# Performance work log

Hardware: AMD Instinct MI355X
Metric: run time of the kernel (lower is better)

Reference implementation:

```python
import jax, jax.numpy as jnp
import numpy as np
import math

B, S, D = 4, 2048, 1024
TAU = 0.5

def setup_inputs() -> dict:
    key = jax.random.key(0)
    ks = jax.random.split(key, 10)
    s = 1.0 / math.sqrt(D)
    return {
        "node_emb": jax.random.normal(ks[0], (B, S, D), jnp.float32),
        "label_emb": jax.random.normal(ks[1], (B, S, D), jnp.float32),
        "Wq": jax.random.uniform(ks[2], (D, D), jnp.float32, -s, s),
        "bq": jax.random.uniform(ks[3], (D,), jnp.float32, -s, s),
        "Wk": jax.random.uniform(ks[4], (D, D), jnp.float32, -s, s),
        "bk": jax.random.uniform(ks[5], (D,), jnp.float32, -s, s),
        "Wv": jax.random.uniform(ks[6], (D, D), jnp.float32, -s, s),
        "bv": jax.random.uniform(ks[7], (D,), jnp.float32, -s, s),
        "Wp": jax.random.uniform(ks[8], (D, D), jnp.float32, -s, s),
        "bp": jax.random.uniform(ks[9], (D,), jnp.float32, -s, s),
    }

def reference(node_emb, label_emb, Wq, bq, Wk, bk, Wv, bv, Wp, bp):
    # Q from label_emb; K, V from node_emb (torch Linear: x @ W.T + b)
    Q = label_emb @ Wq.T + bq          # [B, S, D]
    K = node_emb @ Wk.T + bk           # [B, S, D]
    V = node_emb @ Wv.T + bv           # [B, S, D]
    d = node_emb.shape[-1]
    score = jnp.einsum('bqd,bkd->bqk', Q, K) / jnp.sqrt(jnp.float32(d))
    # causal (lower-triangular) mask, masked_fill(-1e9) BEFORE the tau scale
    causal = jnp.tril(jnp.ones((score.shape[-2], score.shape[-1]), bool))
    score = jnp.where(causal[None, :, :], score, jnp.float32(-1e9))
    attn = jax.nn.softmax(score * TAU, axis=-1)  # [B, S, S]
    # proj_drop is Dropout(0.1); reference runs in eval mode (identity)
    z = jnp.einsum('bqk,bkd->bqd', attn, V)
    return z @ Wp.T + bp
```

## Files before the change

kernel.cpp:

```cpp
#include <hip/hip_runtime.h>
#include <hip/hip_bf16.h>
#include <stdint.h>

using bf16 = __hip_bfloat16;
typedef __bf16 bf16x8 __attribute__((ext_vector_type(8)));
typedef float f32x4 __attribute__((ext_vector_type(4)));
typedef unsigned short u16x8 __attribute__((ext_vector_type(8)));
typedef unsigned short u16x4 __attribute__((ext_vector_type(4)));

#define AS1 __attribute__((address_space(1)))
#define AS3 __attribute__((address_space(3)))

__device__ inline unsigned short f2b(float f) {
    union { __hip_bfloat16 h; unsigned short u; } cv;
    cv.h = __float2bfloat16(f);
    return cv.u;
}

__global__ __launch_bounds__(256) void cvt6(
    const float* __restrict__ i0, const float* __restrict__ i1,
    const float* __restrict__ i2, const float* __restrict__ i3,
    const float* __restrict__ i4, const float* __restrict__ i5,
    u16x8* __restrict__ o0, u16x8* __restrict__ o1,
    u16x8* __restrict__ o2, u16x8* __restrict__ o3,
    u16x8* __restrict__ o4, u16x8* __restrict__ o5,
    long nbig, long nsmall)
{
    const int y = blockIdx.y;
    const float* in = y == 0 ? i0 : (y == 1 ? i1 : (y == 2 ? i2 : (y == 3 ? i3 : (y == 4 ? i4 : i5))));
    u16x8* out = y == 0 ? o0 : (y == 1 ? o1 : (y == 2 ? o2 : (y == 3 ? o3 : (y == 4 ? o4 : o5))));
    const long n8 = (y < 2) ? nbig : nsmall;
    long i = (long)blockIdx.x * blockDim.x + threadIdx.x;
    const long stride = (long)gridDim.x * blockDim.x;
    const float4* in4 = (const float4*)in;
    for (; i < n8; i += stride) {
        float4 x = in4[2 * i], z = in4[2 * i + 1];
        u16x8 o;
        o[0] = f2b(x.x); o[1] = f2b(x.y); o[2] = f2b(x.z); o[3] = f2b(x.w);
        o[4] = f2b(z.x); o[5] = f2b(z.y); o[6] = f2b(z.z); o[7] = f2b(z.w);
        out[i] = o;
    }
}

template <typename T> __device__ inline void storev(T* p, float v);
template <> __device__ inline void storev<float>(float* p, float v) { *p = v; }
template <> __device__ inline void storev<bf16>(bf16* p, float v) { *p = __float2bfloat16(v); }

template <typename OutT, int MODE>
__global__ __launch_bounds__(512, 2) void gemmX(
    const bf16* __restrict__ A0, const bf16* __restrict__ A1,
    const bf16* __restrict__ B0p, const bf16* __restrict__ B1p,
    OutT* __restrict__ C0, OutT* __restrict__ C1,
    const float* __restrict__ bias0, const float* __restrict__ bias1,
    float scale, int lda, int ldb, int ldc, int Kdim,
    long sA, long sB, long sC)
{
    __shared__ __align__(16) char lds[131072];

    const int nwg = gridDim.x;
    const int bid = blockIdx.x;
    const int s = (nwg & 7) ? bid : ((bid & 7) * (nwg >> 3) + (bid >> 3));

    int bm, ccol0, rowB0, seg = 0, bn_s = 0, zidx = 0;
    const bf16 *A, *B;
    OutT* C;
    const float* bias = nullptr;

    if constexpr (MODE == 0) {
        bm = s >> 3; const int bnl = s & 7; seg = bnl >> 2;
        A = A0; B = B0p; rowB0 = bnl * 256;
        C = seg ? C1 : C0; bias = seg ? bias1 : bias0;
        ccol0 = (bnl & 3) * 256;
    } else if constexpr (MODE == 1) {
        seg = s >> 7; const int r = s & 127; bm = r >> 2; const int bn = r & 3;
        A = seg ? A1 : A0; B = seg ? B1p : B0p;
        C = seg ? C1 : C0; bias = seg ? nullptr : bias0;
        rowB0 = bn * 256; ccol0 = bn * 256;
    } else {
        const int z = s / 36, f = s % 36;
        int m = 0;
        while ((m + 1) * (m + 2) / 2 <= f) ++m;
        bm = m; const int bn = f - m * (m + 1) / 2;
        bn_s = bn; zidx = z;
        A = A0 + (long)z * sA; B = B0p + (long)z * sB; C = C0 + (long)z * sC;
        rowB0 = bn * 256; ccol0 = bn * 256;
    }

    const int KT = Kdim >> 6;
    const int NIT = KT >> 1;

    const int tid = threadIdx.x;
    const int lane = tid & 63;
    const int w = tid >> 6;
    const int wm = w >> 2;
    const int wn = w & 3;

    const int rowA0 = bm * 256;

    const int rr  = tid >> 3;
    const int lch = (tid & 7) ^ (rr & 7);
    const bf16* gAt = A + (long)(rowA0 + rr) * lda + lch * 8;
    const bf16* gBt = B + (long)(rowB0 + rr) * ldb + lch * 8;

#define LA(b) (lds + (b) * 65536)
#define LB(b) (lds + 32768 + (b) * 65536)

    auto SG2 = [&](const bf16* g, int ld, char* dst) {
        __builtin_amdgcn_global_load_lds((const AS1 void*)g,
            (AS3 void*)(dst + tid * 16), 16, 0, 0);
        __builtin_amdgcn_global_load_lds((const AS1 void*)(g + (long)64 * ld),
            (AS3 void*)(dst + 8192 + tid * 16), 16, 0, 0);
    };
    auto ST_A = [&](int kt, int half, int b) {
        SG2(gAt + (long)kt * 64 + (long)half * 128 * lda, lda, LA(b) + half * 16384);
    };
    auto ST_B = [&](int kt, int half, int b) {
        SG2(gBt + (long)kt * 64 + (long)half * 128 * ldb, ldb, LB(b) + half * 16384);
    };

    const int abase = (wm * 128 + (lane & 15)) * 128;
    const int bbase = (wn * 64 + (lane & 15)) * 128;
    const int cc0 = (((lane >> 4) << 4)) ^ ((lane & 7) << 4);
    const int cc1 = cc0 ^ 64;

#define RAF(b, mh, mi, kk) (*(const bf16x8*)(LA(b) + abase + (mh)*8192 + (mi)*2048 + ((kk) ? cc1 : cc0)))
#define RBF(b, ni, kk)     (*(const bf16x8*)(LB(b) + bbase + (ni)*2048 + ((kk) ? cc1 : cc0)))

    f32x4 acc[8][4] = {};
    bf16x8 ar[4][2], blo[2][2], bhi[2][2];

#define RD_A2(b, mh, MI0) { ar[MI0][0] = RAF(b, mh, MI0, 0); ar[MI0][1] = RAF(b, mh, MI0, 1); \
                            ar[(MI0)+1][0] = RAF(b, mh, (MI0)+1, 0); ar[(MI0)+1][1] = RAF(b, mh, (MI0)+1, 1); }
#define RD_BLO(b)   { blo[0][0] = RBF(b, 0, 0); blo[0][1] = RBF(b, 0, 1); blo[1][0] = RBF(b, 1, 0); blo[1][1] = RBF(b, 1, 1); }
#define RD_BHI(b)   { bhi[0][0] = RBF(b, 2, 0); bhi[0][1] = RBF(b, 2, 1); bhi[1][0] = RBF(b, 3, 0); bhi[1][1] = RBF(b, 3, 1); }

#define MQ1(MI, bb, MH, NB) { \
    f32x4 t0_ = acc[(MH)*4 + (MI)][(NB)]; \
    t0_ = __builtin_amdgcn_mfma_f32_16x16x32_bf16(ar[MI][0], bb[0][0], t0_, 0, 0, 0); \
    t0_ = __builtin_amdgcn_mfma_f32_16x16x32_bf16(ar[MI][1], bb[0][1], t0_, 0, 0, 0); \
    acc[(MH)*4 + (MI)][(NB)] = t0_; \
    f32x4 t1_ = acc[(MH)*4 + (MI)][(NB) + 1]; \
    t1_ = __builtin_amdgcn_mfma_f32_16x16x32_bf16(ar[MI][0], bb[1][0], t1_, 0, 0, 0); \
    t1_ = __builtin_amdgcn_mfma_f32_16x16x32_bf16(ar[MI][1], bb[1][1], t1_, 0, 0, 0); \
    acc[(MH)*4 + (MI)][(NB) + 1] = t1_; }

#define SCHEDB __builtin_amdgcn_sched_barrier(0)
#define BSYNC { SCHEDB; __builtin_amdgcn_s_barrier(); SCHEDB; }

    auto PRIO1 = [&]() { __builtin_amdgcn_s_setprio(1); };
    auto PRIO0 = [&]() { __builtin_amdgcn_s_setprio(0); };

    ST_A(0, 0, 0); ST_A(0, 1, 0); ST_B(0, 0, 0); ST_B(0, 1, 0);
    ST_B(1, 0, 1); ST_B(1, 1, 1);
    asm volatile("s_waitcnt vmcnt(4)" ::: "memory");
    BSYNC;
    RD_BLO(0); RD_A2(0, 0, 0); RD_A2(0, 0, 2);

    for (int i = 0; i < NIT; ++i) {
        const int t0 = 2 * i;
        const bool last = (i == NIT - 1);

        ST_A(t0 + 1, 0, 1);
        BSYNC; PRIO1();
        RD_BHI(0);
        MQ1(0, blo, 0, 0); MQ1(1, blo, 0, 0); MQ1(2, blo, 0, 0); MQ1(3, blo, 0, 0);
        PRIO0();

        ST_A(t0 + 1, 1, 1);
        BSYNC; PRIO1();
        MQ1(0, bhi, 0, 2); MQ1(1, bhi, 0, 2); MQ1(2, bhi, 0, 2); MQ1(3, bhi, 0, 2);
        RD_A2(0, 1, 0); RD_A2(0, 1, 2);
        PRIO0();

        BSYNC; PRIO1();
        MQ1(0, bhi, 1, 2); MQ1(1, bhi, 1, 2); MQ1(2, bhi, 1, 2); MQ1(3, bhi, 1, 2);
        PRIO0();

        if (!last) { ST_B(t0 + 2, 0, 0); ST_B(t0 + 2, 1, 0);
                     asm volatile("s_waitcnt vmcnt(4)" ::: "memory"); }
        else       { asm volatile("s_waitcnt vmcnt(0)" ::: "memory"); }
        BSYNC; PRIO1();
        MQ1(0, blo, 1, 0); MQ1(1, blo, 1, 0); MQ1(2, blo, 1, 0); MQ1(3, blo, 1, 0);
        RD_BLO(1); RD_A2(1, 0, 0); RD_A2(1, 0, 2);
        PRIO0();

        if (!last) ST_A(t0 + 2, 0, 0);
        BSYNC; PRIO1();
        RD_BHI(1);
        MQ1(0, blo, 0, 0); MQ1(1, blo, 0, 0); MQ1(2, blo, 0, 0); MQ1(3, blo, 0, 0);
        PRIO0();

        if (!last) ST_A(t0 + 2, 1, 0);
        BSYNC; PRIO1();
        MQ1(0, bhi, 0, 2); MQ1(1, bhi, 0, 2); MQ1(2, bhi, 0, 2); MQ1(3, bhi, 0, 2);
        RD_A2(1, 1, 0); RD_A2(1, 1, 2);
        PRIO0();

        BSYNC; PRIO1();
        MQ1(0, bhi, 1, 2); MQ1(1, bhi, 1, 2); MQ1(2, bhi, 1, 2); MQ1(3, bhi, 1, 2);
        PRIO0();

        if (!last) { ST_B(t0 + 3, 0, 1); ST_B(t0 + 3, 1, 1);
                     asm volatile("s_waitcnt vmcnt(4)" ::: "memory"); }
        BSYNC; PRIO1();
        MQ1(0, blo, 1, 0); MQ1(1, blo, 1, 0); MQ1(2, blo, 1, 0); MQ1(3, blo, 1, 0);
        if (!last) { RD_BLO(0); RD_A2(0, 0, 0); RD_A2(0, 0, 2); }
        PRIO0();
    }

    char* tw = lds + w * 16384;
    if constexpr (MODE == 2) {
        const int q = lane >> 4, t = lane & 15;
        const bool diag = (bm == bn_s);
#pragma unroll
        for (int mi = 0; mi < 8; ++mi)
#pragma unroll
            for (int ni = 0; ni < 4; ++ni)
#pragma unroll
                for (int j = 0; j < 4; ++j) {
                    float e = __expf(acc[mi][ni][j] * scale);
                    if (diag) {
                        const int rl = wm * 128 + mi * 16 + q * 4 + j;
                        const int cl = wn * 64 + t + ni * 16;
                        if (cl > rl) e = 0.f;
                    }
                    e = __bfloat162float(__float2bfloat16(e));
                    acc[mi][ni][j] = e;
                }
        float* part = (float*)C1 + ((((long)zidx * 8 + bm) * 32) + bn_s * 4 + wn) * 256;
#pragma unroll
        for (int mi = 0; mi < 8; ++mi) {
            float rs0 = acc[mi][0][0] + acc[mi][1][0] + acc[mi][2][0] + acc[mi][3][0];
            float rs1 = acc[mi][0][1] + acc[mi][1][1] + acc[mi][2][1] + acc[mi][3][1];
            float rs2 = acc[mi][0][2] + acc[mi][1][2] + acc[mi][2][2] + acc[mi][3][2];
            float rs3 = acc[mi][0][3] + acc[mi][1][3] + acc[mi][2][3] + acc[mi][3][3];
#pragma unroll
            for (int d = 1; d < 16; d <<= 1) {
                rs0 += __shfl_xor(rs0, d); rs1 += __shfl_xor(rs1, d);
                rs2 += __shfl_xor(rs2, d); rs3 += __shfl_xor(rs3, d);
            }
            if (t == mi) {
                float4 o; o.x = rs0; o.y = rs1; o.z = rs2; o.w = rs3;
                *(float4*)(part + wm * 128 + mi * 16 + q * 4) = o;
            }
        }
    }
    if (MODE == 1 && seg == 1) {
#pragma unroll
        for (int ni = 0; ni < 4; ++ni) {
            const int cl = ni * 16 + (lane & 15);
            const int sw = 8 * (cl & 7);
#pragma unroll
            for (int mi = 0; mi < 8; ++mi) {
                const int rlb = mi * 16 + ((lane >> 4) << 2);
                u16x4 o;
                o[0] = f2b(acc[mi][ni][0]); o[1] = f2b(acc[mi][ni][1]);
                o[2] = f2b(acc[mi][ni][2]); o[3] = f2b(acc[mi][ni][3]);
                *(u16x4*)(tw + cl * 256 + 2 * (rlb ^ sw)) = o;
            }
        }
        asm volatile("s_waitcnt lgkmcnt(0)" ::: "memory");
        __builtin_amdgcn_sched_barrier(0);
        const int m0 = rowA0 + wm * 128;
        const int z2 = m0 >> 11, mr = m0 & 2047;
        bf16* CT = (bf16*)C + (long)z2 * 2097152 + (long)(ccol0 + wn * 64 + lane) * 2048 + mr;
        const char* tr = tw + lane * 256;
        const int sw2 = lane & 7;
#pragma unroll
        for (int rb = 0; rb < 16; ++rb) {
            u16x8 v = *(const u16x8*)(tr + 16 * (rb ^ sw2));
            *(u16x8*)(CT + 8 * rb) = v;
        }
    } else {
        const float sc2 = (MODE == 2) ? 1.0f : scale;
        const int q = lane >> 4, t = lane & 15;
        const int c0 = ccol0 + wn * 64 + t;
#pragma unroll
        for (int mi = 0; mi < 8; ++mi) {
            char* tm = tw + mi * 2048;
#pragma unroll
            for (int ni = 0; ni < 4; ++ni) {
                const float bv = bias ? bias[c0 + ni * 16] : 0.0f;
                const int cb = (t + 16 * ni) * 2;
#pragma unroll
                for (int j = 0; j < 4; ++j) {
                    const int rl = q * 4 + j;
                    *(bf16*)(tm + rl * 128 + (cb ^ ((rl & 7) << 4))) =
                        __float2bfloat16(acc[mi][ni][j] * sc2 + bv);
                }
            }
        }
        asm volatile("s_waitcnt lgkmcnt(0)" ::: "memory");
        __builtin_amdgcn_sched_barrier(0);
        const int rr2 = lane >> 2, chb = (lane & 3) * 2;
        const int gr0 = rowA0 + wm * 128;
        bf16* Cb = (bf16*)C;
        const int gcb = ccol0 + wn * 64;
#pragma unroll
        for (int mi = 0; mi < 8; ++mi) {
            const char* tm = tw + mi * 2048;
            const long gr = gr0 + mi * 16 + rr2;
#pragma unroll
            for (int k = 0; k < 2; ++k) {
                const int chunk = chb + k;
                u16x8 v = *(const u16x8*)(tm + rr2 * 128 + ((chunk << 4) ^ ((rr2 & 7) << 4)));
                *(u16x8*)(Cb + gr * (long)ldc + gcb + chunk * 8) = v;
            }
        }
    }
#undef RAF
#undef RBF
#undef RD_A2
#undef RD_BLO
#undef RD_BHI
#undef MQ1
#undef LA
#undef LB
}

__global__ __launch_bounds__(512, 2) void pv_bal(
    const bf16* __restrict__ P, const bf16* __restrict__ VT,
    const float* __restrict__ part, float* __restrict__ out,
    const float* __restrict__ bias)
{
    __shared__ __align__(16) char lds[99328];
    float* invl = (float*)(lds + 98304);

    const int nwg = gridDim.x;
    const int bid = blockIdx.x;
    const int s = (bid & 7) * (nwg >> 3) + (bid >> 3);
    const int z = s >> 6, r = s & 63;
    const int pr = r >> 3, bn = r & 7;
    const int bmA = pr, bmB = 15 - pr;

    const bf16* Pz = P + (long)z * 2048 * 2048;
    const bf16* Vz = VT + (long)z * 1024 * 2048;

    const int tid = threadIdx.x;
    const int lane = tid & 63;
    const int w = tid >> 6;
    const int wm = w >> 2, wn = w & 3;
    const int rr = tid >> 3;
    const int lch = (tid & 7) ^ (rr & 7);

    if (tid < 256) {
        const int half = tid >> 7, rloc = tid & 127;
        const int grow = (half ? bmB : bmA) * 128 + rloc;
        const int b256 = grow >> 8, rin = grow & 255;
        const float* pp = part + (((long)z * 8 + b256) * 32) * 256 + rin;
        const int n4 = 4 * (b256 + 1);
        float s0 = 0.f, s1 = 0.f, s2 = 0.f, s3 = 0.f;
        int b4 = 0;
        for (; b4 + 4 <= n4; b4 += 4) {
            s0 += pp[(long)b4 * 256];       s1 += pp[(long)(b4 + 1) * 256];
            s2 += pp[(long)(b4 + 2) * 256]; s3 += pp[(long)(b4 + 3) * 256];
        }
        for (; b4 < n4; ++b4) s0 += pp[(long)b4 * 256];
        invl[tid] = 1.0f / ((s0 + s1) + (s2 + s3));
    }

    const bf16* gBt = Vz + (long)(bn * 128 + rr) * 2048 + lch * 8;
    const bf16* gAtA = Pz + (long)(bmA * 128 + rr) * 2048 + lch * 8;
    const bf16* gAtB = Pz + (long)(bmB * 128 + rr) * 2048 + lch * 8;

    auto SG2 = [&](const bf16* g, char* dst) {
        __builtin_amdgcn_global_load_lds((const AS1 void*)g,
            (AS3 void*)(dst + tid * 16), 16, 0, 0);
        __builtin_amdgcn_global_load_lds((const AS1 void*)(g + (long)64 * 2048),
            (AS3 void*)(dst + 8192 + tid * 16), 16, 0, 0);
    };
    auto ST = [&](const bf16* gAt, int kt, int b) {
        SG2(gAt + (long)kt * 64, lds + b * 32768);
        SG2(gBt + (long)kt * 64, lds + b * 32768 + 16384);
    };

    const int abase0 = (wm * 64 + (lane & 15)) * 128;
    const int bbase0 = 16384 + (wn * 32 + (lane & 15)) * 128;
    const int cc0 = ((lane >> 4) << 4) ^ ((lane & 7) << 4);
    const int cc1 = cc0 ^ 64;

    f32x4 acc[4][2];
    bf16x8 ar[4][2], br[2][2];

    auto RDF = [&](int t) {
        const char* base = lds + (t % 3) * 32768;
#pragma unroll
        for (int mi = 0; mi < 4; ++mi) {
            ar[mi][0] = *(const bf16x8*)(base + abase0 + mi * 2048 + cc0);
            ar[mi][1] = *(const bf16x8*)(base + abase0 + mi * 2048 + cc1);
        }
#pragma unroll
        for (int ni = 0; ni < 2; ++ni) {
            br[ni][0] = *(const bf16x8*)(base + bbase0 + ni * 2048 + cc0);
            br[ni][1] = *(const bf16x8*)(base + bbase0 + ni * 2048 + cc1);
        }
    };
    auto MFMA16 = [&]() {
#pragma unroll
        for (int mi = 0; mi < 4; ++mi)
#pragma unroll
            for (int ni = 0; ni < 2; ++ni) {
                f32x4 t_ = acc[mi][ni];
                t_ = __builtin_amdgcn_mfma_f32_16x16x32_bf16(ar[mi][0], br[ni][0], t_, 0, 0, 0);
                t_ = __builtin_amdgcn_mfma_f32_16x16x32_bf16(ar[mi][1], br[ni][1], t_, 0, 0, 0);
                acc[mi][ni] = t_;
            }
    };
    auto ZERO = [&]() {
#pragma unroll
        for (int mi = 0; mi < 4; ++mi)
#pragma unroll
            for (int ni = 0; ni < 2; ++ni) acc[mi][ni] = f32x4{0.f, 0.f, 0.f, 0.f};
    };
    auto tile_pass = [&](const bf16* gAt, int KT) {
        RDF(0);
        for (int t = 0; t < KT; ++t) {
            if (t + 2 < KT) {
                ST(gAt, t + 2, (t + 2) % 3);
                asm volatile("s_waitcnt vmcnt(4)" ::: "memory");
            } else if (t + 1 < KT) {
                asm volatile("s_waitcnt vmcnt(0)" ::: "memory");
            }
            asm volatile("s_waitcnt lgkmcnt(0)" ::: "memory");
            __builtin_amdgcn_sched_barrier(0);
            __builtin_amdgcn_s_barrier();
            __builtin_amdgcn_sched_barrier(0);
            __builtin_amdgcn_s_setprio(1);
            MFMA16();
            if (t + 1 < KT) RDF(t + 1);
            __builtin_amdgcn_s_setprio(0);
        }
    };
    auto epi = [&](int bm, int invoff) {
        const int q = lane >> 4, t16 = lane & 15;
        const int c0 = bn * 128 + wn * 32 + t16;
        float* op = out + ((long)z * 2048 + (long)bm * 128) * 1024;
#pragma unroll
        for (int mi = 0; mi < 4; ++mi)
#pragma unroll
            for (int j = 0; j < 4; ++j) {
                const int rl = wm * 64 + mi * 16 + q * 4 + j;
                const float iv = invl[invoff + rl];
#pragma unroll
                for (int ni = 0; ni < 2; ++ni) {
                    const int c = c0 + ni * 16;
                    op[(long)rl * 1024 + c] = acc[mi][ni][j] * iv + bias[c];
                }
            }
    };

    const int KTA = 2 * (bmA + 1), KTB = 2 * (bmB + 1);

    ST(gAtA, 0, 0); ST(gAtA, 1, 1);
    asm volatile("s_waitcnt vmcnt(4)" ::: "memory");
    __builtin_amdgcn_s_barrier();
    __builtin_amdgcn_sched_barrier(0);
    ZERO();
    tile_pass(gAtA, KTA);

    ST(gAtB, 0, 0); ST(gAtB, 1, 1);
    epi(bmA, 0);
    asm volatile("s_waitcnt vmcnt(0)" ::: "memory");
    __builtin_amdgcn_s_barrier();
    __builtin_amdgcn_sched_barrier(0);
    ZERO();
    tile_pass(gAtB, KTB);
    epi(bmB, 128);
}

extern "C" void kernel_launch(void* const* d_in, const int* in_sizes, int n_in,
                              void* d_out, int out_size, void* d_ws, size_t ws_size,
                              hipStream_t stream) {
    const int B = 4, S = 2048, D = 1024;
    const long MD = (long)B * S * D;
    const float scale = 0.5f / 32.0f;

    const float* node  = (const float*)d_in[0];
    const float* label = (const float*)d_in[1];
    const float* Wq = (const float*)d_in[2];
    const float* bq = (const float*)d_in[3];
    const float* Wk = (const float*)d_in[4];
    const float* bk = (const float*)d_in[5];
    const float* Wv = (const float*)d_in[6];
    const float* bv = (const float*)d_in[7];
    const float* Wp = (const float*)d_in[8];
    const float* bp = (const float*)d_in[9];
    float* out = (float*)d_out;

    char* ws = (char*)d_ws;
    bf16* nodeb  = (bf16*)(ws);
    bf16* VTb    = nodeb;
    bf16* labelb = (bf16*)(ws + 16777216);
    bf16* Wqb = (bf16*)(ws + 33554432);
    bf16* Wkb = (bf16*)(ws + 35651584);
    bf16* Wvb = (bf16*)(ws + 37748736);
    bf16* Wpb = (bf16*)(ws + 39845888);
    bf16* Qb  = (bf16*)(ws + 41943040);
    bf16* Kb  = (bf16*)(ws + 58720256);
    bf16* Vb  = (bf16*)(ws + 75497472);
    float* partial = (float*)(ws + 75497472);
    bf16* SP  = (bf16*)(ws + 92274688);
    if (ws_size < 125829120UL) return;

    cvt6<<<dim3(512, 6), 256, 0, stream>>>(
        node, label, Wq, Wk, Wv, Wp,
        (u16x8*)nodeb, (u16x8*)labelb, (u16x8*)Wqb, (u16x8*)Wkb, (u16x8*)Wvb, (u16x8*)Wpb,
        MD / 8, (long)D * D / 8);

    gemmX<bf16, 0><<<256, 512, 0, stream>>>(
        nodeb, nullptr, Wkb, nullptr, Kb, Vb, bk, bv,
        1.0f, D, D, D, D, 0, 0, 0);

    gemmX<bf16, 1><<<256, 512, 0, stream>>>(
        labelb, Vb, Wqb, Wpb, Qb, VTb, bq, nullptr,
        1.0f, D, D, D, D, 0, 0, 0);

    gemmX<bf16, 2><<<144, 512, 0, stream>>>(
        Qb, nullptr, Kb, (bf16*)nullptr, SP, (bf16*)partial, nullptr, nullptr,
        scale, D, D, S, D, (long)S * D, (long)S * D, (long)S * S);

    pv_bal<<<256, 512, 0, stream>>>(SP, VTb, partial, out, bp);
}
```

Measured before the change: 152.2 us.

## Replace causal score GEMM with dedicated 256x128-tile kernel over 288 blocks

Measured after the change: 160.6 us. 5.6% more time.

```diff
diff --git a/kernel.cpp b/kernel.cpp
--- a/kernel.cpp
+++ b/kernel.cpp
@@ -61,7 +61,7 @@
     const int bid = blockIdx.x;
     const int s = (nwg & 7) ? bid : ((bid & 7) * (nwg >> 3) + (bid >> 3));
 
-    int bm, ccol0, rowB0, seg = 0, bn_s = 0, zidx = 0;
+    int bm, ccol0, rowB0, seg = 0;
     const bf16 *A, *B;
     OutT* C;
     const float* bias = nullptr;
@@ -71,18 +71,10 @@
         A = A0; B = B0p; rowB0 = bnl * 256;
         C = seg ? C1 : C0; bias = seg ? bias1 : bias0;
         ccol0 = (bnl & 3) * 256;
-    } else if constexpr (MODE == 1) {
+    } else {
         seg = s >> 7; const int r = s & 127; bm = r >> 2; const int bn = r & 3;
         A = seg ? A1 : A0; B = seg ? B1p : B0p;
         C = seg ? C1 : C0; bias = seg ? nullptr : bias0;
-        rowB0 = bn * 256; ccol0 = bn * 256;
-    } else {
-        const int z = s / 36, f = s % 36;
-        int m = 0;
-        while ((m + 1) * (m + 2) / 2 <= f) ++m;
-        bm = m; const int bn = f - m * (m + 1) / 2;
-        bn_s = bn; zidx = z;
-        A = A0 + (long)z * sA; B = B0p + (long)z * sB; C = C0 + (long)z * sC;
         rowB0 = bn * 256; ccol0 = bn * 256;
     }
 
@@ -209,42 +201,6 @@
     }
 
     char* tw = lds + w * 16384;
-    if constexpr (MODE == 2) {
-        const int q = lane >> 4, t = lane & 15;
-        const bool diag = (bm == bn_s);
-#pragma unroll
-        for (int mi = 0; mi < 8; ++mi)
-#pragma unroll
-            for (int ni = 0; ni < 4; ++ni)
-#pragma unroll
-                for (int j = 0; j < 4; ++j) {
-                    float e = __expf(acc[mi][ni][j] * scale);
-                    if (diag) {
-                        const int rl = wm * 128 + mi * 16 + q * 4 + j;
-                        const int cl = wn * 64 + t + ni * 16;
-                        if (cl > rl) e = 0.f;
-                    }
-                    e = __bfloat162float(__float2bfloat16(e));
-                    acc[mi][ni][j] = e;
-                }
-        float* part = (float*)C1 + ((((long)zidx * 8 + bm) * 32) + bn_s * 4 + wn) * 256;
-#pragma unroll
-        for (int mi = 0; mi < 8; ++mi) {
-            float rs0 = acc[mi][0][0] + acc[mi][1][0] + acc[mi][2][0] + acc[mi][3][0];
-            float rs1 = acc[mi][0][1] + acc[mi][1][1] + acc[mi][2][1] + acc[mi][3][1];
-            float rs2 = acc[mi][0][2] + acc[mi][1][2] + acc[mi][2][2] + acc[mi][3][2];
-            float rs3 = acc[mi][0][3] + acc[mi][1][3] + acc[mi][2][3] + acc[mi][3][3];
-#pragma unroll
-            for (int d = 1; d < 16; d <<= 1) {
-                rs0 += __shfl_xor(rs0, d); rs1 += __shfl_xor(rs1, d);
-                rs2 += __shfl_xor(rs2, d); rs3 += __shfl_xor(rs3, d);
-            }
-            if (t == mi) {
-                float4 o; o.x = rs0; o.y = rs1; o.z = rs2; o.w = rs3;
-                *(float4*)(part + wm * 128 + mi * 16 + q * 4) = o;
-            }
-        }
-    }
     if (MODE == 1 && seg == 1) {
 #pragma unroll
         for (int ni = 0; ni < 4; ++ni) {
@@ -272,7 +228,6 @@
             *(u16x8*)(CT + 8 * rb) = v;
         }
     } else {
-        const float sc2 = (MODE == 2) ? 1.0f : scale;
         const int q = lane >> 4, t = lane & 15;
         const int c0 = ccol0 + wn * 64 + t;
 #pragma unroll
@@ -286,7 +241,7 @@
                 for (int j = 0; j < 4; ++j) {
                     const int rl = q * 4 + j;
                     *(bf16*)(tm + rl * 128 + (cb ^ ((rl & 7) << 4))) =
-                        __float2bfloat16(acc[mi][ni][j] * sc2 + bv);
+                        __float2bfloat16(acc[mi][ni][j] * scale + bv);
                 }
             }
         }
@@ -306,6 +261,197 @@
                 u16x8 v = *(const u16x8*)(tm + rr2 * 128 + ((chunk << 4) ^ ((rr2 & 7) << 4)));
                 *(u16x8*)(Cb + gr * (long)ldc + gcb + chunk * 8) = v;
             }
+        }
+    }
+#undef RAF
+#undef RBF
+#undef RD_A2
+#undef RD_BLO
+#undef RD_BHI
+#undef MQ1
+#undef LA
+#undef LB
+}
+
+__global__ __launch_bounds__(512, 2) void score128(
+    const bf16* __restrict__ Qp, const bf16* __restrict__ Kp,
+    bf16* __restrict__ SP, float* __restrict__ part, float scale)
+{
+    __shared__ __align__(16) char lds[98304];
+
+    const int bid = blockIdx.x;
+    const int s = (bid & 7) * 36 + (bid >> 3);
+    const int z = s / 72, f = s % 72;
+    int bm = 0;
+    while ((bm + 1) * (bm + 2) <= f) ++bm;
+    const int bn = f - bm * (bm + 1);
+
+    const bf16* A = Qp + (long)z * 2048 * 1024;
+    const bf16* B = Kp + (long)z * 2048 * 1024;
+    bf16* C = SP + (long)z * 2048 * 2048;
+    const int rowA0 = bm * 256, rowB0 = bn * 128;
+
+    const int tid = threadIdx.x;
+    const int lane = tid & 63;
+    const int w = tid >> 6;
+    const int wm = w >> 1, wn = w & 1;
+
+    const int rr  = tid >> 3;
+    const int lch = (tid & 7) ^ (rr & 7);
+    const bf16* gAt = A + (long)(rowA0 + rr) * 1024 + lch * 8;
+    const bf16* gBt = B + (long)(rowB0 + rr) * 1024 + lch * 8;
+
+#define LA(b) (lds + (b) * 49152)
+#define LB(b) (lds + 32768 + (b) * 49152)
+
+    auto SG2 = [&](const bf16* g, char* dst) {
+        __builtin_amdgcn_global_load_lds((const AS1 void*)g,
+            (AS3 void*)(dst + tid * 16), 16, 0, 0);
+        __builtin_amdgcn_global_load_lds((const AS1 void*)(g + (long)64 * 1024),
+            (AS3 void*)(dst + 8192 + tid * 16), 16, 0, 0);
+    };
+    auto ST_A = [&](int kt, int half, int b) {
+        SG2(gAt + (long)kt * 64 + (long)half * 128 * 1024, LA(b) + half * 16384);
+    };
+    auto ST_B1 = [&](int kt, int b) {
+        SG2(gBt + (long)kt * 64, LB(b));
+    };
+
+    const int abase = (wm * 64 + (lane & 15)) * 128;
+    const int bbase = (wn * 64 + (lane & 15)) * 128;
+    const int cc0 = (((lane >> 4) << 4)) ^ ((lane & 7) << 4);
+    const int cc1 = cc0 ^ 64;
+
+#define RAF(b, mi, kk) (*(const bf16x8*)(LA(b) + abase + (mi)*2048 + ((kk) ? cc1 : cc0)))
+#define RBF(b, ni, kk) (*(const bf16x8*)(LB(b) + bbase + (ni)*2048 + ((kk) ? cc1 : cc0)))
+
+    f32x4 acc[4][4] = {};
+    bf16x8 ar[4][2], blo[2][2], bhi[2][2];
+
+#define RD_A2(b, MI0) { ar[MI0][0] = RAF(b, MI0, 0); ar[MI0][1] = RAF(b, MI0, 1); \
+                        ar[(MI0)+1][0] = RAF(b, (MI0)+1, 0); ar[(MI0)+1][1] = RAF(b, (MI0)+1, 1); }
+#define RD_BLO(b)   { blo[0][0] = RBF(b, 0, 0); blo[0][1] = RBF(b, 0, 1); blo[1][0] = RBF(b, 1, 0); blo[1][1] = RBF(b, 1, 1); }
+#define RD_BHI(b)   { bhi[0][0] = RBF(b, 2, 0); bhi[0][1] = RBF(b, 2, 1); bhi[1][0] = RBF(b, 3, 0); bhi[1][1] = RBF(b, 3, 1); }
+
+#define MQ1(MI, bb, NB) { \
+    f32x4 t0_ = acc[MI][(NB)]; \
+    t0_ = __builtin_amdgcn_mfma_f32_16x16x32_bf16(ar[MI][0], bb[0][0], t0_, 0, 0, 0); \
+    t0_ = __builtin_amdgcn_mfma_f32_16x16x32_bf16(ar[MI][1], bb[0][1], t0_, 0, 0, 0); \
+    acc[MI][(NB)] = t0_; \
+    f32x4 t1_ = acc[MI][(NB) + 1]; \
+    t1_ = __builtin_amdgcn_mfma_f32_16x16x32_bf16(ar[MI][0], bb[1][0], t1_, 0, 0, 0); \
+    t1_ = __builtin_amdgcn_mfma_f32_16x16x32_bf16(ar[MI][1], bb[1][1], t1_, 0, 0, 0); \
+    acc[MI][(NB) + 1] = t1_; }
+
+#define SCHEDB __builtin_amdgcn_sched_barrier(0)
+#define WAIT_LGKM0 { asm volatile("s_waitcnt lgkmcnt(0)" ::: "memory"); SCHEDB; }
+#define WAIT_LGKM4 { asm volatile("s_waitcnt lgkmcnt(4)" ::: "memory"); SCHEDB; }
+
+    auto BAR = [&]() { __builtin_amdgcn_s_barrier(); SCHEDB; };
+    auto PRIO1 = [&]() { __builtin_amdgcn_s_setprio(1); };
+    auto PRIO0 = [&]() { __builtin_amdgcn_s_setprio(0); };
+
+    ST_A(0, 0, 0); ST_A(0, 1, 0); ST_B1(0, 0);
+    ST_A(1, 0, 1); ST_A(1, 1, 1); ST_B1(1, 1);
+    asm volatile("s_waitcnt vmcnt(6)" ::: "memory");
+    BAR();
+
+    const int NIT = 8;
+    for (int i = 0; i < NIT; ++i) {
+        const int t0 = 2 * i;
+        const bool last = (i == NIT - 1);
+
+        RD_BLO(0); RD_A2(0, 0); RD_A2(0, 2); SCHEDB; RD_BHI(0);
+        BAR(); WAIT_LGKM4; PRIO1();
+        MQ1(0, blo, 0); MQ1(1, blo, 0); MQ1(2, blo, 0); MQ1(3, blo, 0);
+        PRIO0(); BAR();
+
+        if (!last) { ST_A(t0 + 2, 0, 0); ST_A(t0 + 2, 1, 0);
+                     asm volatile("s_waitcnt vmcnt(4)" ::: "memory"); }
+        else       { asm volatile("s_waitcnt vmcnt(0)" ::: "memory"); }
+        BAR(); WAIT_LGKM0; PRIO1();
+        MQ1(0, bhi, 2); MQ1(1, bhi, 2); MQ1(2, bhi, 2); MQ1(3, bhi, 2);
+        PRIO0(); BAR();
+
+        RD_BLO(1); RD_A2(1, 0); RD_A2(1, 2); SCHEDB; RD_BHI(1);
+        if (!last) ST_B1(t0 + 2, 0);
+        BAR(); WAIT_LGKM4; PRIO1();
+        MQ1(0, blo, 0); MQ1(1, blo, 0); MQ1(2, blo, 0); MQ1(3, blo, 0);
+        PRIO0(); BAR();
+
+        if (!last) { ST_A(t0 + 3, 0, 1); ST_A(t0 + 3, 1, 1); ST_B1(t0 + 3, 1);
+                     asm volatile("s_waitcnt vmcnt(6)" ::: "memory"); }
+        BAR(); WAIT_LGKM0; PRIO1();
+        MQ1(0, bhi, 2); MQ1(1, bhi, 2); MQ1(2, bhi, 2); MQ1(3, bhi, 2);
+        PRIO0(); BAR();
+    }
+
+    const int q = lane >> 4, t = lane & 15;
+    const bool diag = (bn >> 1) == bm;
+    const int delta = (bn - 2 * bm) * 128;
+#pragma unroll
+    for (int mi = 0; mi < 4; ++mi)
+#pragma unroll
+        for (int ni = 0; ni < 4; ++ni)
+#pragma unroll
+            for (int j = 0; j < 4; ++j) {
+                float e = __expf(acc[mi][ni][j] * scale);
+                if (diag) {
+                    const int rl = wm * 64 + mi * 16 + q * 4 + j;
+                    const int cl = wn * 64 + t + ni * 16;
+                    if (delta + cl > rl) e = 0.f;
+                }
+                e = __bfloat162float(__float2bfloat16(e));
+                acc[mi][ni][j] = e;
+            }
+
+    float* pp = part + ((((long)z * 8 + bm) * 32) + bn * 2 + wn) * 256;
+#pragma unroll
+    for (int mi = 0; mi < 4; ++mi) {
+        float rs0 = acc[mi][0][0] + acc[mi][1][0] + acc[mi][2][0] + acc[mi][3][0];
+        float rs1 = acc[mi][0][1] + acc[mi][1][1] + acc[mi][2][1] + acc[mi][3][1];
+        float rs2 = acc[mi][0][2] + acc[mi][1][2] + acc[mi][2][2] + acc[mi][3][2];
+        float rs3 = acc[mi][0][3] + acc[mi][1][3] + acc[mi][2][3] + acc[mi][3][3];
+#pragma unroll
+        for (int d = 1; d < 16; d <<= 1) {
+            rs0 += __shfl_xor(rs0, d); rs1 += __shfl_xor(rs1, d);
+            rs2 += __shfl_xor(rs2, d); rs3 += __shfl_xor(rs3, d);
+        }
+        if (t == mi) {
+            float4 o; o.x = rs0; o.y = rs1; o.z = rs2; o.w = rs3;
+            *(float4*)(pp + wm * 64 + mi * 16 + q * 4) = o;
+        }
+    }
+
+    char* tw = lds + w * 8192;
+#pragma unroll
+    for (int mi = 0; mi < 4; ++mi) {
+        char* tm = tw + mi * 2048;
+#pragma unroll
+        for (int ni = 0; ni < 4; ++ni) {
+            const int cb = (t + 16 * ni) * 2;
+#pragma unroll
+            for (int j = 0; j < 4; ++j) {
+                const int rl = q * 4 + j;
+                *(bf16*)(tm + rl * 128 + (cb ^ ((rl & 7) << 4))) =
+                    __float2bfloat16(acc[mi][ni][j]);
+            }
+        }
+    }
+    asm volatile("s_waitcnt lgkmcnt(0)" ::: "memory");
+    __builtin_amdgcn_sched_barrier(0);
+    const int rr2 = lane >> 2, chb = (lane & 3) * 2;
+    const int gr0 = rowA0 + wm * 64;
+    const int gcb = rowB0 + wn * 64;
+#pragma unroll
+    for (int mi = 0; mi < 4; ++mi) {
+        const char* tm = tw + mi * 2048;
+        const long gr = gr0 + mi * 16 + rr2;
+#pragma unroll
+        for (int k = 0; k < 2; ++k) {
+            const int chunk = chb + k;
+            u16x8 v = *(const u16x8*)(tm + rr2 * 128 + ((chunk << 4) ^ ((rr2 & 7) << 4)));
+            *(u16x8*)(C + gr * 2048 + gcb + chunk * 8) = v;
         }
     }
 #undef RAF
@@ -515,9 +661,7 @@
         labelb, Vb, Wqb, Wpb, Qb, VTb, bq, nullptr,
         1.0f, D, D, D, D, 0, 0, 0);
 
-    gemmX<bf16, 2><<<144, 512, 0, stream>>>(
-        Qb, nullptr, Kb, (bf16*)nullptr, SP, (bf16*)partial, nullptr, nullptr,
-        scale, D, D, S, D, (long)S * D, (long)S * D, (long)S * S);
+    score128<<<288, 512, 0, stream>>>(Qb, Kb, SP, partial, scale);
 
     pv_bal<<<256, 512, 0, stream>>>(SP, VTb, partial, out, bp);
 }
```
